# Kernel optimization log

Hardware: AMD Instinct MI355X
Metric: run time of the kernel (lower is better)

The kernel has to match this reference:

```python
import jax, jax.numpy as jnp
import numpy as np

HIDDEN = 64
NHEADS = 8
HEAD_DIM = HIDDEN // NHEADS
N_EDGES = 800000
N_NODES = 50000


def setup_inputs() -> dict:
    key = jax.random.key(0)
    k1, k2, k3, k4 = jax.random.split(key, 4)
    keys = jax.random.normal(k1, (N_EDGES, HIDDEN), dtype=jnp.float32)
    queries = jax.random.normal(k2, (N_EDGES, HIDDEN), dtype=jnp.float32)
    values = jax.random.normal(k3, (N_EDGES, HIDDEN), dtype=jnp.float32)
    dst = jax.random.randint(k4, (N_EDGES,), 0, N_NODES, dtype=jnp.int32)
    return {"keys": keys, "queries": queries, "values": values,
            "dst": dst, "num_nodes": N_NODES}


def reference(keys, queries, values, dst, num_nodes):
    E = keys.shape[0]
    temp = HIDDEN ** (-0.5)
    # reshape to (E, H, D) multi-head layout
    k = keys.reshape(E, NHEADS, HEAD_DIM)
    q = queries.reshape(E, NHEADS, HEAD_DIM)
    v = values.reshape(E, NHEADS, HEAD_DIM)
    # edge-wise dot-product score per head, scaled, then LeakyReLU(0.2)
    scores = jnp.sum(k * q, axis=-1) * temp            # (E, H)
    scores = jnp.where(scores >= 0, scores, 0.2 * scores)
    # segment softmax over edges grouped by destination node (dgl.ops.edge_softmax)
    smax = jax.ops.segment_max(scores, dst, num_segments=num_nodes)  # (N, H)
    smax = jnp.where(jnp.isfinite(smax), smax, 0.0)    # nodes with no in-edges
    ex = jnp.exp(scores - smax[dst])                   # (E, H)
    denom = jax.ops.segment_sum(ex, dst, num_segments=num_nodes)    # (N, H)
    weights = ex / denom[dst]                          # (E, H)
    # dropout p=0.0 -> identity; mask/bias are None -> skipped
    weighted = weights[..., None] * v                  # (E, H, D)
    # scatter-sum to destination nodes (dgl.ops.copy_e_sum)
    out = jax.ops.segment_sum(weighted, dst, num_segments=num_nodes)  # (N, H, D)
    return out.reshape(num_nodes, HIDDEN)
```

## Files before the change

kernel.cpp:

```cpp
#include <hip/hip_runtime.h>

#define HIDDEN 64
#define NHEADS 8

typedef float f4 __attribute__((ext_vector_type(4)));


__global__ void hist_kernel(const int* __restrict__ dst, int* __restrict__ counts, int E) {
    int i = blockIdx.x * blockDim.x + threadIdx.x;
    if (i < E) atomicAdd(&counts[dst[i]], 1);
}

__global__ void scan1_kernel(const int* __restrict__ counts, int* __restrict__ offsets,
                             int* __restrict__ partials, int N) {
    int tid = threadIdx.x, lane = tid & 63, wid = tid >> 6;
    int i = blockIdx.x * 256 + tid;
    int x0 = (i < N) ? counts[i] : 0;
    int x = x0;
    #pragma unroll
    for (int off = 1; off < 64; off <<= 1) {
        int y = __shfl_up(x, off);
        if (lane >= off) x += y;
    }
    __shared__ int wsum[4];
    if (lane == 63) wsum[wid] = x;
    __syncthreads();
    if (tid == 0) {
        int s = 0;
        #pragma unroll
        for (int w2 = 0; w2 < 4; ++w2) { int t = wsum[w2]; wsum[w2] = s; s += t; }
        partials[blockIdx.x] = s;
    }
    __syncthreads();
    if (i < N) offsets[i] = wsum[wid] + (x - x0);
}

__global__ void scan2_kernel(int* __restrict__ partials, int PB) {
    int tid = threadIdx.x, lane = tid & 63, wid = tid >> 6;
    int x0 = (tid < PB) ? partials[tid] : 0;
    int x = x0;
    #pragma unroll
    for (int off = 1; off < 64; off <<= 1) {
        int y = __shfl_up(x, off);
        if (lane >= off) x += y;
    }
    __shared__ int wsum[4];
    if (lane == 63) wsum[wid] = x;
    __syncthreads();
    if (tid == 0) {
        int s = 0;
        #pragma unroll
        for (int w2 = 0; w2 < 4; ++w2) { int t = wsum[w2]; wsum[w2] = s; s += t; }
    }
    __syncthreads();
    if (tid < PB) partials[tid] = wsum[wid] + (x - x0);
}

__global__ void scan3_kernel(int* __restrict__ offsets, int* __restrict__ cursor,
                             const int* __restrict__ partials, int N, int E) {
    int i = blockIdx.x * 256 + threadIdx.x;
    if (i < N) {
        int o = offsets[i] + partials[blockIdx.x];
        offsets[i] = o;
        cursor[i] = o;
    }
    if (i == 0) offsets[N] = E;
}

__global__ void scatter_score_kernel(const float* __restrict__ k,
                                     const float* __restrict__ q,
                                     const int* __restrict__ dst,
                                     int* __restrict__ cursor,
                                     int* __restrict__ edge_ids,
                                     float* __restrict__ ex8, int E) {
    int tid = blockIdx.x * blockDim.x + threadIdx.x;
    int e = tid >> 3, h = tid & 7;
    if (e >= E) return;
    int lane = threadIdx.x & 63;

    const f4* kp = (const f4*)(k + (size_t)e * HIDDEN + h * 8);
    const f4* qp = (const f4*)(q + (size_t)e * HIDDEN + h * 8);
    f4 k0 = __builtin_nontemporal_load(kp);
    f4 k1 = __builtin_nontemporal_load(kp + 1);
    f4 q0 = __builtin_nontemporal_load(qp);
    f4 q1 = __builtin_nontemporal_load(qp + 1);
    float pr = k0.x * q0.x + k0.y * q0.y + k0.z * q0.z + k0.w * q0.w +
               k1.x * q1.x + k1.y * q1.y + k1.z * q1.z + k1.w * q1.w;
    float sc = pr * 0.125f;
    sc = (sc >= 0.f) ? sc : 0.2f * sc;
    float exv = __expf(sc);

    int pos = 0;
    if (h == 0) pos = atomicAdd(&cursor[dst[e]], 1);
    pos = __shfl(pos, lane & ~7);
    if (h == 0) edge_ids[pos] = e;
    ex8[(size_t)pos * 8 + h] = exv;
}

__global__ void gat_gather_kernel(const float* __restrict__ v,
                                  const float* __restrict__ ex8,
                                  const int* __restrict__ offsets,
                                  const int* __restrict__ edge_ids,
                                  float* __restrict__ out, int N) {
    int wgid = blockIdx.x * (blockDim.x >> 6) + (threadIdx.x >> 6);
    if (wgid >= N) return;
    int lane = threadIdx.x & 63;
    int h = lane >> 3;
    int start = offsets[wgid], end = offsets[wgid + 1];
    if (end <= start) {
        out[(size_t)wgid * HIDDEN + lane] = 0.f;
        return;
    }
    float acc = 0.f, den = 0.f;

    for (int cbase = start; cbase < end; cbase += 16) {
        int idx[16];
        int eid[16];
        float w[16], vv[16];
        #pragma unroll
        for (int jj = 0; jj < 16; ++jj) {
            int i0 = cbase + jj;
            idx[jj] = (i0 < end) ? i0 : (end - 1);
        }
        #pragma unroll
        for (int jj = 0; jj < 16; ++jj) eid[jj] = edge_ids[idx[jj]];
        #pragma unroll
        for (int jj = 0; jj < 16; ++jj) {
            w[jj]  = ex8[(size_t)idx[jj] * 8 + h];
            vv[jj] = v[(size_t)eid[jj] * HIDDEN + lane];
        }
        #pragma unroll
        for (int jj = 0; jj < 16; ++jj) {
            float m = (cbase + jj < end) ? w[jj] : 0.f;
            acc = fmaf(m, vv[jj], acc);
            den += m;
        }
    }
    out[(size_t)wgid * HIDDEN + lane] = acc / den;
}

extern "C" void kernel_launch(void* const* d_in, const int* in_sizes, int n_in,
                              void* d_out, int out_size, void* d_ws, size_t ws_size,
                              hipStream_t stream) {
    const float* keys    = (const float*)d_in[0];
    const float* queries = (const float*)d_in[1];
    const float* values  = (const float*)d_in[2];
    const int*   dst     = (const int*)d_in[3];
    int E = in_sizes[0] / HIDDEN;
    int N = out_size / HIDDEN;

    char* w = (char*)d_ws;
    int* counts   = (int*)w;
    int* offsets  = counts + N;
    int* cursor   = offsets + N + 1;
    int* partials = cursor + N;
    size_t used = (size_t)(3 * N + 1 + 256) * sizeof(int);
    used = (used + 15) & ~(size_t)15;
    int* edge_ids = (int*)(w + used);
    used += (size_t)E * sizeof(int);
    used = (used + 15) & ~(size_t)15;
    float* ex8 = (float*)(w + used);
    float* out = (float*)d_out;

    hipMemsetAsync(counts, 0, (size_t)N * sizeof(int), stream);

    int threads = 256;
    int eb = (E + threads - 1) / threads;
    int nb256 = (N + 255) / 256;

    hist_kernel<<<eb, threads, 0, stream>>>(dst, counts, E);
    scan1_kernel<<<nb256, 256, 0, stream>>>(counts, offsets, partials, N);
    scan2_kernel<<<1, 256, 0, stream>>>(partials, nb256);
    scan3_kernel<<<nb256, 256, 0, stream>>>(offsets, cursor, partials, N, E);

    int ehb = ((E * NHEADS) + threads - 1) / threads;
    scatter_score_kernel<<<ehb, threads, 0, stream>>>(keys, queries, dst,
                                                      cursor, edge_ids, ex8, E);

    int wavesPerBlock = threads / 64;
    int gb = (N + wavesPerBlock - 1) / wavesPerBlock;
    gat_gather_kernel<<<gb, threads, 0, stream>>>(values, ex8, offsets,
                                                  edge_ids, out, N);
}
```

Baseline: 204.4 us.

## Batch key/query loads per thread in a grid-stride score-scatter kernel

The score/scatter kernel becomes a persistent grid-stride loop over 2048-item chunks on a fixed 2048-block grid. Each thread issues all eight key loads for its chunk up front, then the query loads and dot products, and only then does the atomic cursor increments and scatter stores. The aim is more memory-level parallelism and less per-block launch overhead on this bandwidth-bound streaming pass over keys and queries. The cost is higher register pressure from holding sixteen f4 values, and the serialized atomic phase at the end of each chunk.

New measurement: 214.5 us. 1.05x slower.

```diff
diff --git a/kernel.cpp b/kernel.cpp
--- a/kernel.cpp
+++ b/kernel.cpp
@@ -67,34 +67,60 @@
     if (i == 0) offsets[N] = E;
 }
 
-__global__ void scatter_score_kernel(const float* __restrict__ k,
-                                     const float* __restrict__ q,
-                                     const int* __restrict__ dst,
-                                     int* __restrict__ cursor,
-                                     int* __restrict__ edge_ids,
-                                     float* __restrict__ ex8, int E) {
-    int tid = blockIdx.x * blockDim.x + threadIdx.x;
-    int e = tid >> 3, h = tid & 7;
-    if (e >= E) return;
-    int lane = threadIdx.x & 63;
-
-    const f4* kp = (const f4*)(k + (size_t)e * HIDDEN + h * 8);
-    const f4* qp = (const f4*)(q + (size_t)e * HIDDEN + h * 8);
-    f4 k0 = __builtin_nontemporal_load(kp);
-    f4 k1 = __builtin_nontemporal_load(kp + 1);
-    f4 q0 = __builtin_nontemporal_load(qp);
-    f4 q1 = __builtin_nontemporal_load(qp + 1);
-    float pr = k0.x * q0.x + k0.y * q0.y + k0.z * q0.z + k0.w * q0.w +
-               k1.x * q1.x + k1.y * q1.y + k1.z * q1.z + k1.w * q1.w;
-    float sc = pr * 0.125f;
-    sc = (sc >= 0.f) ? sc : 0.2f * sc;
-    float exv = __expf(sc);
-
-    int pos = 0;
-    if (h == 0) pos = atomicAdd(&cursor[dst[e]], 1);
-    pos = __shfl(pos, lane & ~7);
-    if (h == 0) edge_ids[pos] = e;
-    ex8[(size_t)pos * 8 + h] = exv;
+__global__ __launch_bounds__(256) void
+scatter_score_kernel(const float* __restrict__ k,
+                     const float* __restrict__ q,
+                     const int* __restrict__ dst,
+                     int* __restrict__ cursor,
+                     int* __restrict__ edge_ids,
+                     float* __restrict__ ex8, int E) {
+    int nItems = E * NHEADS;
+    int nch = (nItems + 2047) >> 11;
+    int tid = threadIdx.x;
+    int h = tid & 7;
+    int lane = tid & 63;
+
+    for (int c = blockIdx.x; c < nch; c += gridDim.x) {
+        int cbase = c << 11;
+        bool full = (cbase + 2048 <= nItems);
+
+        f4 ka[16];
+        #pragma unroll
+        for (int i = 0; i < 8; ++i) {
+            int item = cbase + i * 256 + tid;
+            if (!full && item >= nItems) item = nItems - 1;
+            const f4* kp = (const f4*)(k + ((size_t)item << 3));
+            ka[2 * i]     = __builtin_nontemporal_load(kp);
+            ka[2 * i + 1] = __builtin_nontemporal_load(kp + 1);
+        }
+        __builtin_amdgcn_sched_barrier(0);
+        float exv[8];
+        #pragma unroll
+        for (int i = 0; i < 8; ++i) {
+            int item = cbase + i * 256 + tid;
+            if (!full && item >= nItems) item = nItems - 1;
+            const f4* qp = (const f4*)(q + ((size_t)item << 3));
+            f4 q0 = __builtin_nontemporal_load(qp);
+            f4 q1 = __builtin_nontemporal_load(qp + 1);
+            f4 k0 = ka[2 * i], k1 = ka[2 * i + 1];
+            float pr = k0.x * q0.x + k0.y * q0.y + k0.z * q0.z + k0.w * q0.w +
+                       k1.x * q1.x + k1.y * q1.y + k1.z * q1.z + k1.w * q1.w;
+            float sc = pr * 0.125f;
+            sc = (sc >= 0.f) ? sc : 0.2f * sc;
+            exv[i] = __expf(sc);
+        }
+        #pragma unroll
+        for (int i = 0; i < 8; ++i) {
+            int item = cbase + i * 256 + tid;
+            if (!full && item >= nItems) break;
+            int e = item >> 3;
+            int pos = 0;
+            if (h == 0) pos = atomicAdd(&cursor[dst[e]], 1);
+            pos = __shfl(pos, lane & ~7);
+            if (h == 0) edge_ids[pos] = e;
+            ex8[(size_t)pos * 8 + h] = exv[i];
+        }
+    }
 }
 
 __global__ void gat_gather_kernel(const float* __restrict__ v,
@@ -173,9 +199,8 @@
     scan2_kernel<<<1, 256, 0, stream>>>(partials, nb256);
     scan3_kernel<<<nb256, 256, 0, stream>>>(offsets, cursor, partials, N, E);
 
-    int ehb = ((E * NHEADS) + threads - 1) / threads;
-    scatter_score_kernel<<<ehb, threads, 0, stream>>>(keys, queries, dst,
-                                                      cursor, edge_ids, ex8, E);
+    scatter_score_kernel<<<2048, threads, 0, stream>>>(keys, queries, dst,
+                                                       cursor, edge_ids, ex8, E);
 
     int wavesPerBlock = threads / 64;
     int gb = (N + wavesPerBlock - 1) / wavesPerBlock;
```
